# Kernel tuning notes

Measured on AMD Instinct MI355X. Metric: run time of the kernel, lower is better.

Reference implementation:

```python
import jax, jax.numpy as jnp
import numpy as np

H = 1024        # hidden_size
NH = 16         # num heads
HD = H // NH    # head dim = 64
B, S = 2, 2048


def _linear_params(key, fan_in, fan_out):
    k1, k2 = jax.random.split(key)
    bound = 1.0 / np.sqrt(fan_in)
    w = jax.random.uniform(k1, (fan_in, fan_out), jnp.float32, -bound, bound)
    b = jax.random.uniform(k2, (fan_out,), jnp.float32, -bound, bound)
    return w, b


def setup_inputs() -> dict:
    key = jax.random.key(0)
    ks = jax.random.split(key, 10)
    hidden_states = jax.random.normal(ks[0], (B, S, H), jnp.float32)
    topic_states = jax.random.normal(ks[1], (B, H), jnp.float32)
    attention_mask = jnp.zeros((B, 1, 1, S), jnp.float32)
    Wq, bq = _linear_params(ks[2], H, H)
    Wk, bk = _linear_params(ks[3], H, H)
    Wv, bv = _linear_params(ks[4], H, H)
    Wtp, btp = _linear_params(ks[5], H, H)
    Wta, bta = _linear_params(ks[6], H, H)
    Wd, bd = _linear_params(ks[7], H, H)
    ln_g = jnp.ones((H,), jnp.float32)
    ln_b = jnp.zeros((H,), jnp.float32)
    return {
        "hidden_states": hidden_states, "topic_states": topic_states,
        "attention_mask": attention_mask,
        "Wq": Wq, "bq": bq, "Wk": Wk, "bk": bk, "Wv": Wv, "bv": bv,
        "Wtp": Wtp, "btp": btp, "Wta": Wta, "bta": bta,
        "Wd": Wd, "bd": bd, "ln_g": ln_g, "ln_b": ln_b,
    }


def reference(hidden_states, topic_states, attention_mask,
              Wq, bq, Wk, bk, Wv, bv, Wtp, btp, Wta, bta, Wd, bd, ln_g, ln_b):
    # topic gating: two linears on [B,H], broadcast over seq
    topic_proj = topic_states @ Wtp + btp
    topic_att = topic_proj @ Wta + bta                     # [B,H]
    gate = jax.nn.sigmoid(topic_att)[:, None, :]           # [B,1,H]

    q = hidden_states @ Wq + bq                            # [B,S,H]
    k = (hidden_states @ Wk + bk) * gate                   # sigmoid-gated keys
    v = hidden_states @ Wv + bv

    def split_heads(x):  # [B,S,H] -> [B,NH,S,HD]
        return x.reshape(B, S, NH, HD).transpose(0, 2, 1, 3)

    qh, kh, vh = split_heads(q), split_heads(k), split_heads(v)

    scores = jnp.einsum('bhqd,bhkd->bhqk', qh, kh) / np.sqrt(HD).astype(np.float32)
    scores = scores + attention_mask                       # additive mask
    probs = jax.nn.softmax(scores, axis=-1)                # dropout = identity (eval)
    ctx = jnp.einsum('bhqk,bhkd->bhqd', probs, vh)
    ctx = ctx.transpose(0, 2, 1, 3).reshape(B, S, H)

    out = ctx @ Wd + bd                                    # dense + (eval) dropout
    x = out + hidden_states                                # residual
    mu = jnp.mean(x, axis=-1, keepdims=True)
    var = jnp.mean(jnp.square(x - mu), axis=-1, keepdims=True)
    return (x - mu) * jax.lax.rsqrt(var + 1e-5) * ln_g + ln_b
```

## Files before the change

kernel.cpp:

```cpp
#include <hip/hip_runtime.h>

typedef unsigned short u16;
typedef unsigned int   u32;
typedef __attribute__((ext_vector_type(4)))  float f32x4;
typedef __attribute__((ext_vector_type(16))) float f32x16;
typedef __attribute__((ext_vector_type(8)))  __bf16 bf16x8;
typedef __attribute__((ext_vector_type(8)))  u16  u16x8;
typedef __attribute__((ext_vector_type(4)))  u16  u16x4;

#define HDIM 1024
#define SEQ  2048
#define NB   2
#define MROWS 4096
#define QSCALE 0.18033688011111793f
#define LOG2E  1.4426950408889634f
#define TOPK 64
#define TOPC 16

__device__ __forceinline__ u16 f2bf(float f) {
  u32 u = __float_as_uint(f);
  u32 r = u + 0x7FFFu + ((u >> 16) & 1u);
  return (u16)(r >> 16);
}

__device__ __forceinline__ u32 pkbf(float a, float b) {
  union { __bf16 h[2]; u32 w; } u;
  u.h[0] = (__bf16)a; u.h[1] = (__bf16)b;
  return u.w;
}

__device__ __forceinline__ void gload_lds16(const void* gp, void* lp) {
  __builtin_amdgcn_global_load_lds(
      (const __attribute__((address_space(1))) void*)gp,
      (__attribute__((address_space(3))) void*)lp, 16, 0, 0);
}

__global__ void wt_bf16_kernel(const float* __restrict__ w0, const float* __restrict__ w1,
                               const float* __restrict__ w2, const float* __restrict__ w3,
                               u16* __restrict__ out) {
  const float* W = (blockIdx.z == 0) ? w0 : (blockIdx.z == 1) ? w1 : (blockIdx.z == 2) ? w2 : w3;
  u16* Wt = out + (size_t)blockIdx.z * HDIM * HDIM;
  __shared__ float t[32][33];
  const int k0 = blockIdx.x * 32, n0 = blockIdx.y * 32;
  const int tx = threadIdx.x, ty = threadIdx.y;
#pragma unroll
  for (int j = 0; j < 32; j += 8)
    t[ty + j][tx] = W[(size_t)(k0 + ty + j) * HDIM + n0 + tx];
  __syncthreads();
#pragma unroll
  for (int j = 0; j < 32; j += 8)
    Wt[(size_t)(n0 + ty + j) * HDIM + k0 + tx] = f2bf(t[tx][ty + j]);
}

__global__ void cvt_bf16_kernel(const float* __restrict__ in, u16* __restrict__ out) {
  const size_t i = (size_t)blockIdx.x * 256 + threadIdx.x;
  f32x4 v = *(const f32x4*)(in + i * 4);
  u16x4 o;
#pragma unroll
  for (int e = 0; e < 4; ++e) o[e] = f2bf(v[e]);
  *(u16x4*)(out + i * 4) = o;
}

__global__ void maskcvt_kernel(const float* __restrict__ m, float* __restrict__ o) {
  const int i = blockIdx.x * 256 + threadIdx.x;
  o[i] = m[i] * LOG2E;
}

__global__ void topic_partial_kernel(const float* __restrict__ in, const float* __restrict__ W,
                                     float* __restrict__ part) {
  const int c = blockIdx.x;
  const int b = blockIdx.y;
  const int t = threadIdx.x;
  const float* inb = in + b * HDIM + c * TOPK;
  f32x4 acc = {};
#pragma unroll 8
  for (int k = 0; k < TOPK; ++k) {
    const f32x4 w4 = *(const f32x4*)(W + (size_t)(c * TOPK + k) * HDIM + t * 4);
    acc += inb[k] * w4;
  }
  *(f32x4*)(part + ((size_t)(b * TOPC + c)) * HDIM + t * 4) = acc;
}

__global__ void topic_reduce_kernel(const float* __restrict__ part, const float* __restrict__ bias,
                                    float* __restrict__ out, int sigmoid_mode) {
  const int b = blockIdx.y;
  const int n = blockIdx.x * 256 + threadIdx.x;
  float s = bias[n];
#pragma unroll
  for (int c = 0; c < TOPC; ++c) s += part[((size_t)(b * TOPC + c)) * HDIM + n];
  out[b * HDIM + n] = sigmoid_mode ? (1.f / (1.f + __expf(-s))) : s;
}

template <int MODE>
__global__ __launch_bounds__(256, 2)
void gemm_kernel(const u16* __restrict__ A, const u16* __restrict__ Wt,
                 const float* __restrict__ b0, const float* __restrict__ b1,
                 const float* __restrict__ b2, const float* __restrict__ gate,
                 const float* __restrict__ resid,
                 u16* __restrict__ outb, float* __restrict__ outf) {
  const int n0 = blockIdx.x * 128;
  const int m0 = blockIdx.y * 128;
  const int z = blockIdx.z;
  const u16* W = Wt + (size_t)z * (HDIM * HDIM);
  const float* bias = (MODE == 0) ? (z == 0 ? b0 : (z == 1 ? b1 : b2)) : b0;

  __shared__ __align__(16) u16 Alds[128 * 64];
  __shared__ __align__(16) u16 Blds[128 * 64];

  const int tid = threadIdx.x;
  const int lane = tid & 63;
  const int w = tid >> 6;
  const int wm = w >> 1, wn = w & 1;
  const int srow = tid >> 3, sslot = tid & 7;

  f32x4 acc[4][4] = {};

  for (int k0 = 0; k0 < HDIM; k0 += 64) {
    __syncthreads();
#pragma unroll
    for (int j = 0; j < 4; ++j) {
      const int row = j * 32 + srow;
      const int gs = (sslot ^ (row & 7)) * 8;
      gload_lds16(A + (size_t)(m0 + row) * HDIM + k0 + gs, Alds + j * 2048 + w * 512);
      gload_lds16(W + (size_t)(n0 + row) * HDIM + k0 + gs, Blds + j * 2048 + w * 512);
    }
    __syncthreads();
#pragma unroll
    for (int kk = 0; kk < 2; ++kk) {
      const int slot = ((((kk << 2) + (lane >> 4)) ^ (lane & 7)) << 3);
      bf16x8 af[4], bfr[4];
#pragma unroll
      for (int i = 0; i < 4; ++i) {
        af[i]  = *(const bf16x8*)(&Alds[(wm * 64 + i * 16 + (lane & 15)) * 64 + slot]);
        bfr[i] = *(const bf16x8*)(&Blds[(wn * 64 + i * 16 + (lane & 15)) * 64 + slot]);
      }
#pragma unroll
      for (int i = 0; i < 4; ++i)
#pragma unroll
        for (int jn = 0; jn < 4; ++jn)
          acc[i][jn] = __builtin_amdgcn_mfma_f32_16x16x32_bf16(af[i], bfr[jn], acc[i][jn], 0, 0, 0);
    }
  }

  const int rbase = (lane >> 4) << 2;
#pragma unroll
  for (int i = 0; i < 4; ++i) {
#pragma unroll
    for (int jn = 0; jn < 4; ++jn) {
      const int n = n0 + wn * 64 + jn * 16 + (lane & 15);
      const float bv = bias[n];
#pragma unroll
      for (int r = 0; r < 4; ++r) {
        const int m = m0 + wm * 64 + i * 16 + rbase + r;
        float v = acc[i][jn][r] + bv;
        if (MODE == 0) {
          if (z == 0) v *= QSCALE;
          if (z == 1) v *= gate[(m >> 11) * HDIM + n];
          outb[(size_t)z * MROWS * HDIM + (size_t)m * HDIM + n] = f2bf(v);
        } else {
          v += resid[(size_t)m * HDIM + n];
          outf[(size_t)m * HDIM + n] = v;
        }
      }
    }
  }
}

__global__ __launch_bounds__(256, 2)
void attn_kernel(const u16* __restrict__ Q, const u16* __restrict__ K,
                 const u16* __restrict__ V, const float* __restrict__ mask2,
                 u16* __restrict__ O) {
  const int q0 = blockIdx.x * 128;
  const int h = blockIdx.y;
  const int b = blockIdx.z;
  const size_t base = ((size_t)b * SEQ) * HDIM + h * 64;
  const int tid = threadIdx.x, lane = tid & 63, w = tid >> 6;
  const int hh = lane >> 5;
  const int ql = lane & 31;
  const int srow = tid >> 3, sslot = tid & 7;

  __shared__ __align__(16) u16 Kss[2][64 * 64];
  __shared__ __align__(16) u16 Vts[2][64 * 64];

  bf16x8 Qf[4];
  {
    const u16* qp = Q + base + (size_t)(q0 + w * 32 + ql) * HDIM;
#pragma unroll
    for (int ds = 0; ds < 4; ++ds)
      Qf[ds] = *(const bf16x8*)(qp + ds * 16 + hh * 8);
  }

  float m_run = -1e30f, l_run = 0.f;
  f32x16 accA = {}, accB = {};

  {
#pragma unroll
    for (int c = 0; c < 2; ++c) {
      const int i2 = c * 4 + w;
      const int row = i2 * 8 + (lane >> 3);
      const int sl = lane & 7;
      gload_lds16(K + base + (size_t)row * HDIM + ((sl ^ (row & 7)) * 8),
                  &Kss[0][i2 * 512]);
    }
    u16x8 vr[2];
#pragma unroll
    for (int jj = 0; jj < 2; ++jj)
      vr[jj] = *(const u16x8*)(V + base + (size_t)(jj * 32 + srow) * HDIM + sslot * 8);
#pragma unroll
    for (int jj = 0; jj < 2; ++jj) {
      const int kr = jj * 32 + srow;
#pragma unroll
      for (int e = 0; e < 8; ++e) {
        const int d = sslot * 8 + e;
        Vts[0][d * 64 + ((((kr >> 3) ^ (d & 7) ^ ((d >> 3) & 7))) << 3) + (kr & 7)] = vr[jj][e];
      }
    }
  }
  __syncthreads();

  for (int t = 0; t < SEQ / 64; ++t) {
    const int cur = t & 1;
    const int kvt0 = t * 64;
    u16x8 vr[2];
    if (t + 1 < SEQ / 64) {
#pragma unroll
      for (int jj = 0; jj < 2; ++jj)
        vr[jj] = *(const u16x8*)(V + base + (size_t)(kvt0 + 64 + jj * 32 + srow) * HDIM + sslot * 8);
#pragma unroll
      for (int c = 0; c < 2; ++c) {
        const int i2 = c * 4 + w;
        const int row = i2 * 8 + (lane >> 3);
        const int sl = lane & 7;
        gload_lds16(K + base + (size_t)(kvt0 + 64 + row) * HDIM + ((sl ^ (row & 7)) * 8),
                    &Kss[cur ^ 1][i2 * 512]);
      }
    }

#pragma unroll
    for (int kvb = 0; kvb < 2; ++kvb) {
      f32x16 sv = {};
#pragma unroll
      for (int ds = 0; ds < 4; ++ds) {
        const bf16x8 kf = *(const bf16x8*)(
            &Kss[cur][(kvb * 32 + ql) * 64 + (((ds * 2 + hh) ^ (ql & 7)) << 3)]);
        sv = __builtin_amdgcn_mfma_f32_32x32x16_bf16(kf, Qf[ds], sv, 0, 0, 0);
      }
      f32x4 m4[4];
      {
        const float* mrow = mask2 + (size_t)b * SEQ + kvt0 + kvb * 32 + hh * 4;
#pragma unroll
        for (int g = 0; g < 4; ++g) m4[g] = *(const f32x4*)(mrow + g * 8);
      }
      f32x16 s_;
#pragma unroll
      for (int j = 0; j < 16; ++j) s_[j] = sv[j] + m4[j >> 2][j & 3];

      float mx0 = fmaxf(fmaxf(s_[0], s_[1]), fmaxf(s_[2], s_[3]));
      float mx1 = fmaxf(fmaxf(s_[4], s_[5]), fmaxf(s_[6], s_[7]));
      float mx2 = fmaxf(fmaxf(s_[8], s_[9]), fmaxf(s_[10], s_[11]));
      float mx3 = fmaxf(fmaxf(s_[12], s_[13]), fmaxf(s_[14], s_[15]));
      float mx = fmaxf(fmaxf(mx0, mx1), fmaxf(mx2, mx3));
      mx = fmaxf(mx, __shfl_xor(mx, 32));

      if (!__all(mx <= m_run + 8.f)) {
        const float mnew = fmaxf(m_run, mx);
        const float corr = __builtin_amdgcn_exp2f(m_run - mnew);
        m_run = mnew;
        l_run *= corr;
#pragma unroll
        for (int j = 0; j < 16; ++j) {
          const float cj = __shfl(corr, (j & 3) + 8 * (j >> 2) + 4 * hh);
          accA[j] *= cj; accB[j] *= cj;
        }
      }

      f32x16 p_;
#pragma unroll
      for (int j = 0; j < 16; ++j) p_[j] = __builtin_amdgcn_exp2f(s_[j] - m_run);
      {
        float r0 = (p_[0] + p_[1]) + (p_[2] + p_[3]);
        float r1 = (p_[4] + p_[5]) + (p_[6] + p_[7]);
        float r2 = (p_[8] + p_[9]) + (p_[10] + p_[11]);
        float r3 = (p_[12] + p_[13]) + (p_[14] + p_[15]);
        float rs = (r0 + r1) + (r2 + r3);
        rs += __shfl_xor(rs, 32);
        l_run += rs;
      }

#pragma unroll
      for (int s2 = 0; s2 < 2; ++s2) {
        const u32 a0 = pkbf(p_[s2 * 8 + 0], p_[s2 * 8 + 1]);
        const u32 a1 = pkbf(p_[s2 * 8 + 2], p_[s2 * 8 + 3]);
        const u32 b0v = pkbf(p_[s2 * 8 + 4], p_[s2 * 8 + 5]);
        const u32 b1v = pkbf(p_[s2 * 8 + 6], p_[s2 * 8 + 7]);
        const u32 sd0 = hh ? a0 : b0v, sd1 = hh ? a1 : b1v;
        const u32 r0 = (u32)__shfl_xor((int)sd0, 32);
        const u32 r1 = (u32)__shfl_xor((int)sd1, 32);
        union { u32 u[4]; bf16x8 v; } pu;
        pu.u[0] = hh ? r0 : a0;  pu.u[1] = hh ? r1 : a1;
        pu.u[2] = hh ? b0v : r0; pu.u[3] = hh ? b1v : r1;
        const int ks = kvb * 4 + s2 * 2 + hh;
#pragma unroll
        for (int dt = 0; dt < 2; ++dt) {
          const int d = dt * 32 + ql;
          const bf16x8 vf = *(const bf16x8*)(
              &Vts[cur][d * 64 + ((ks ^ (d & 7) ^ ((d >> 3) & 7)) << 3)]);
          if (dt == 0) accA = __builtin_amdgcn_mfma_f32_32x32x16_bf16(pu.v, vf, accA, 0, 0, 0);
          else         accB = __builtin_amdgcn_mfma_f32_32x32x16_bf16(pu.v, vf, accB, 0, 0, 0);
        }
      }
    }

    if (t + 1 < SEQ / 64) {
#pragma unroll
      for (int jj = 0; jj < 2; ++jj) {
        const int kr = jj * 32 + srow;
#pragma unroll
        for (int e = 0; e < 8; ++e) {
          const int d = sslot * 8 + e;
          Vts[cur ^ 1][d * 64 + ((((kr >> 3) ^ (d & 7) ^ ((d >> 3) & 7))) << 3) + (kr & 7)] = vr[jj][e];
        }
      }
    }
    __syncthreads();
  }

  const float linv = 1.f / l_run;
#pragma unroll
  for (int j = 0; j < 16; ++j) {
    const int rq = (j & 3) + 8 * (j >> 2) + 4 * hh;
    const float lj = __shfl(linv, rq);
    const size_t orow = base + (size_t)(q0 + w * 32 + rq) * HDIM;
    O[orow + ql]      = f2bf(accA[j] * lj);
    O[orow + 32 + ql] = f2bf(accB[j] * lj);
  }
}

__global__ void ln_kernel(const float* __restrict__ x, const float* __restrict__ g,
                          const float* __restrict__ bb, float* __restrict__ out) {
  const int row = blockIdx.x;
  const int tid = threadIdx.x;
  const f32x4 v = *(const f32x4*)(x + (size_t)row * HDIM + tid * 4);
  float s = v[0] + v[1] + v[2] + v[3];
  float s2 = v[0] * v[0] + v[1] * v[1] + v[2] * v[2] + v[3] * v[3];
#pragma unroll
  for (int o = 1; o < 64; o <<= 1) { s += __shfl_xor(s, o); s2 += __shfl_xor(s2, o); }
  __shared__ float rs[4], rs2[4];
  if ((tid & 63) == 0) { rs[tid >> 6] = s; rs2[tid >> 6] = s2; }
  __syncthreads();
  s = rs[0] + rs[1] + rs[2] + rs[3];
  s2 = rs2[0] + rs2[1] + rs2[2] + rs2[3];
  const float mu = s * (1.f / HDIM);
  const float var = s2 * (1.f / HDIM) - mu * mu;
  const float inv = rsqrtf(var + 1e-5f);
  f32x4 o4;
#pragma unroll
  for (int e = 0; e < 4; ++e) {
    const int c = tid * 4 + e;
    o4[e] = (v[e] - mu) * inv * g[c] + bb[c];
  }
  *(f32x4*)(out + (size_t)row * HDIM + tid * 4) = o4;
}

extern "C" void kernel_launch(void* const* d_in, const int* in_sizes, int n_in,
                              void* d_out, int out_size, void* d_ws, size_t ws_size,
                              hipStream_t stream) {
  const float* hidden = (const float*)d_in[0];
  const float* topic  = (const float*)d_in[1];
  const float* mask   = (const float*)d_in[2];
  const float* Wq  = (const float*)d_in[3];  const float* bq  = (const float*)d_in[4];
  const float* Wk  = (const float*)d_in[5];  const float* bk  = (const float*)d_in[6];
  const float* Wv  = (const float*)d_in[7];  const float* bv  = (const float*)d_in[8];
  const float* Wtp = (const float*)d_in[9];  const float* btp = (const float*)d_in[10];
  const float* Wta = (const float*)d_in[11]; const float* bta = (const float*)d_in[12];
  const float* Wd  = (const float*)d_in[13]; const float* bd  = (const float*)d_in[14];
  const float* lng = (const float*)d_in[15]; const float* lnb = (const float*)d_in[16];
  float* out = (float*)d_out;

  char* ws = (char*)d_ws;
  u16* hs_bf  = (u16*)(ws);
  u16* WtAll  = (u16*)(ws + (size_t)(8u << 20));
  u16* qkv    = (u16*)(ws + (size_t)(16u << 20));
  u16* ctx    = (u16*)(ws + (size_t)(40u << 20));
  float* xbuf = (float*)(ws + (size_t)(16u << 20));
  float* tproj = (float*)(ws + (size_t)(48u << 20));
  float* tgate = (float*)(ws + (size_t)(48u << 20) + 8192);
  float* mask2 = (float*)(ws + (size_t)(48u << 20));
  float* tpart = (float*)(ws + (size_t)(16u << 20));

  wt_bf16_kernel<<<dim3(32, 32, 4), dim3(32, 8), 0, stream>>>(Wq, Wk, Wv, Wd, WtAll);
  cvt_bf16_kernel<<<4096, 256, 0, stream>>>(hidden, hs_bf);
  topic_partial_kernel<<<dim3(TOPC, NB), 256, 0, stream>>>(topic, Wtp, tpart);
  topic_reduce_kernel<<<dim3(4, NB), 256, 0, stream>>>(tpart, btp, tproj, 0);
  topic_partial_kernel<<<dim3(TOPC, NB), 256, 0, stream>>>(tproj, Wta, tpart);
  topic_reduce_kernel<<<dim3(4, NB), 256, 0, stream>>>(tpart, bta, tgate, 1);
  gemm_kernel<0><<<dim3(8, 32, 3), 256, 0, stream>>>(hs_bf, WtAll, bq, bk, bv, tgate,
                                                     nullptr, qkv, nullptr);
  maskcvt_kernel<<<16, 256, 0, stream>>>(mask, mask2);
  attn_kernel<<<dim3(16, 16, NB), 256, 0, stream>>>(qkv, qkv + (size_t)MROWS * HDIM,
                                                    qkv + 2 * (size_t)MROWS * HDIM, mask2, ctx);
  gemm_kernel<1><<<dim3(8, 32, 1), 256, 0, stream>>>(ctx, WtAll + 3 * (size_t)HDIM * HDIM,
                                                     bd, nullptr, nullptr, nullptr, hidden,
                                                     nullptr, xbuf);
  ln_kernel<<<4096, 256, 0, stream>>>(xbuf, lng, lnb, out);
}
```

Measured before the change: 163.9 us.

## Process full 64-key tile per softmax step, fold mask scaling, add MFMA priority

```diff
diff --git a/kernel.cpp b/kernel.cpp
--- a/kernel.cpp
+++ b/kernel.cpp
@@ -59,11 +59,6 @@
 #pragma unroll
   for (int e = 0; e < 4; ++e) o[e] = f2bf(v[e]);
   *(u16x4*)(out + i * 4) = o;
-}
-
-__global__ void maskcvt_kernel(const float* __restrict__ m, float* __restrict__ o) {
-  const int i = blockIdx.x * 256 + threadIdx.x;
-  o[i] = m[i] * LOG2E;
 }
 
 __global__ void topic_partial_kernel(const float* __restrict__ in, const float* __restrict__ W,
@@ -168,7 +163,7 @@
 
 __global__ __launch_bounds__(256, 2)
 void attn_kernel(const u16* __restrict__ Q, const u16* __restrict__ K,
-                 const u16* __restrict__ V, const float* __restrict__ mask2,
+                 const u16* __restrict__ V, const float* __restrict__ mask,
                  u16* __restrict__ O) {
   const int q0 = blockIdx.x * 128;
   const int h = blockIdx.y;
@@ -236,63 +231,82 @@
       }
     }
 
+    f32x16 sv[2] = {{}, {}};
+    __builtin_amdgcn_s_setprio(1);
+#pragma unroll
+    for (int ds = 0; ds < 4; ++ds) {
+      const int xo = (((ds * 2 + hh) ^ (ql & 7)) << 3);
+      const bf16x8 kf0 = *(const bf16x8*)(&Kss[cur][(ql) * 64 + xo]);
+      const bf16x8 kf1 = *(const bf16x8*)(&Kss[cur][(32 + ql) * 64 + xo]);
+      sv[0] = __builtin_amdgcn_mfma_f32_32x32x16_bf16(kf0, Qf[ds], sv[0], 0, 0, 0);
+      sv[1] = __builtin_amdgcn_mfma_f32_32x32x16_bf16(kf1, Qf[ds], sv[1], 0, 0, 0);
+    }
+    __builtin_amdgcn_s_setprio(0);
+
+    f32x4 m4[2][4];
+    {
+      const float* mrow = mask + (size_t)b * SEQ + kvt0 + hh * 4;
+#pragma unroll
+      for (int g = 0; g < 4; ++g) {
+        m4[0][g] = *(const f32x4*)(mrow + g * 8);
+        m4[1][g] = *(const f32x4*)(mrow + 32 + g * 8);
+      }
+    }
+    f32x16 s_[2];
+#pragma unroll
+    for (int kvb = 0; kvb < 2; ++kvb)
+#pragma unroll
+      for (int j = 0; j < 16; ++j)
+        s_[kvb][j] = fmaf(m4[kvb][j >> 2][j & 3], LOG2E, sv[kvb][j]);
+
+    float t8[8];
+#pragma unroll
+    for (int j = 0; j < 8; ++j)
+      t8[j] = fmaxf(fmaxf(s_[0][j], s_[0][j + 8]), fmaxf(s_[1][j], s_[1][j + 8]));
+    float t4a = fmaxf(t8[0], t8[1]), t4b = fmaxf(t8[2], t8[3]);
+    float t4c = fmaxf(t8[4], t8[5]), t4d = fmaxf(t8[6], t8[7]);
+    float mx = fmaxf(fmaxf(t4a, t4b), fmaxf(t4c, t4d));
+    mx = fmaxf(mx, __shfl_xor(mx, 32));
+
+    if (!__all(mx <= m_run + 8.f)) {
+      const float mnew = fmaxf(m_run, mx);
+      const float corr = __builtin_amdgcn_exp2f(m_run - mnew);
+      m_run = mnew;
+      l_run *= corr;
+#pragma unroll
+      for (int j = 0; j < 16; ++j) {
+        const float cj = __shfl(corr, (j & 3) + 8 * (j >> 2) + 4 * hh);
+        accA[j] *= cj; accB[j] *= cj;
+      }
+    }
+
+    f32x16 p_[2];
+#pragma unroll
+    for (int kvb = 0; kvb < 2; ++kvb)
+#pragma unroll
+      for (int j = 0; j < 16; ++j)
+        p_[kvb][j] = __builtin_amdgcn_exp2f(s_[kvb][j] - m_run);
+    {
+      float r8[8];
+#pragma unroll
+      for (int j = 0; j < 8; ++j)
+        r8[j] = (p_[0][j] + p_[0][j + 8]) + (p_[1][j] + p_[1][j + 8]);
+      float ra = (r8[0] + r8[1]) + (r8[2] + r8[3]);
+      float rb = (r8[4] + r8[5]) + (r8[6] + r8[7]);
+      float rs = ra + rb;
+      rs += __shfl_xor(rs, 32);
+      l_run += rs;
+    }
+
+    __builtin_amdgcn_s_setprio(1);
 #pragma unroll
     for (int kvb = 0; kvb < 2; ++kvb) {
-      f32x16 sv = {};
-#pragma unroll
-      for (int ds = 0; ds < 4; ++ds) {
-        const bf16x8 kf = *(const bf16x8*)(
-            &Kss[cur][(kvb * 32 + ql) * 64 + (((ds * 2 + hh) ^ (ql & 7)) << 3)]);
-        sv = __builtin_amdgcn_mfma_f32_32x32x16_bf16(kf, Qf[ds], sv, 0, 0, 0);
-      }
-      f32x4 m4[4];
-      {
-        const float* mrow = mask2 + (size_t)b * SEQ + kvt0 + kvb * 32 + hh * 4;
-#pragma unroll
-        for (int g = 0; g < 4; ++g) m4[g] = *(const f32x4*)(mrow + g * 8);
-      }
-      f32x16 s_;
-#pragma unroll
-      for (int j = 0; j < 16; ++j) s_[j] = sv[j] + m4[j >> 2][j & 3];
-
-      float mx0 = fmaxf(fmaxf(s_[0], s_[1]), fmaxf(s_[2], s_[3]));
-      float mx1 = fmaxf(fmaxf(s_[4], s_[5]), fmaxf(s_[6], s_[7]));
-      float mx2 = fmaxf(fmaxf(s_[8], s_[9]), fmaxf(s_[10], s_[11]));
-      float mx3 = fmaxf(fmaxf(s_[12], s_[13]), fmaxf(s_[14], s_[15]));
-      float mx = fmaxf(fmaxf(mx0, mx1), fmaxf(mx2, mx3));
-      mx = fmaxf(mx, __shfl_xor(mx, 32));
-
-      if (!__all(mx <= m_run + 8.f)) {
-        const float mnew = fmaxf(m_run, mx);
-        const float corr = __builtin_amdgcn_exp2f(m_run - mnew);
-        m_run = mnew;
-        l_run *= corr;
-#pragma unroll
-        for (int j = 0; j < 16; ++j) {
-          const float cj = __shfl(corr, (j & 3) + 8 * (j >> 2) + 4 * hh);
-          accA[j] *= cj; accB[j] *= cj;
-        }
-      }
-
-      f32x16 p_;
-#pragma unroll
-      for (int j = 0; j < 16; ++j) p_[j] = __builtin_amdgcn_exp2f(s_[j] - m_run);
-      {
-        float r0 = (p_[0] + p_[1]) + (p_[2] + p_[3]);
-        float r1 = (p_[4] + p_[5]) + (p_[6] + p_[7]);
-        float r2 = (p_[8] + p_[9]) + (p_[10] + p_[11]);
-        float r3 = (p_[12] + p_[13]) + (p_[14] + p_[15]);
-        float rs = (r0 + r1) + (r2 + r3);
-        rs += __shfl_xor(rs, 32);
-        l_run += rs;
-      }
-
 #pragma unroll
       for (int s2 = 0; s2 < 2; ++s2) {
-        const u32 a0 = pkbf(p_[s2 * 8 + 0], p_[s2 * 8 + 1]);
-        const u32 a1 = pkbf(p_[s2 * 8 + 2], p_[s2 * 8 + 3]);
-        const u32 b0v = pkbf(p_[s2 * 8 + 4], p_[s2 * 8 + 5]);
-        const u32 b1v = pkbf(p_[s2 * 8 + 6], p_[s2 * 8 + 7]);
+        const u32 a0 = pkbf(p_[kvb][s2 * 8 + 0], p_[kvb][s2 * 8 + 1]);
+        const u32 a1 = pkbf(p_[kvb][s2 * 8 + 2], p_[kvb][s2 * 8 + 3]);
+        const u32 b0v = pkbf(p_[kvb][s2 * 8 + 4], p_[kvb][s2 * 8 + 5]);
+        const u32 b1v = pkbf(p_[kvb][s2 * 8 + 6], p_[kvb][s2 * 8 + 7]);
         const u32 sd0 = hh ? a0 : b0v, sd1 = hh ? a1 : b1v;
         const u32 r0 = (u32)__shfl_xor((int)sd0, 32);
         const u32 r1 = (u32)__shfl_xor((int)sd1, 32);
@@ -310,6 +324,7 @@
         }
       }
     }
+    __builtin_amdgcn_s_setprio(0);
 
     if (t + 1 < SEQ / 64) {
 #pragma unroll
@@ -385,7 +400,6 @@
   float* xbuf = (float*)(ws + (size_t)(16u << 20));
   float* tproj = (float*)(ws + (size_t)(48u << 20));
   float* tgate = (float*)(ws + (size_t)(48u << 20) + 8192);
-  float* mask2 = (float*)(ws + (size_t)(48u << 20));
   float* tpart = (float*)(ws + (size_t)(16u << 20));
 
   wt_bf16_kernel<<<dim3(32, 32, 4), dim3(32, 8), 0, stream>>>(Wq, Wk, Wv, Wd, WtAll);
@@ -396,9 +410,8 @@
   topic_reduce_kernel<<<dim3(4, NB), 256, 0, stream>>>(tpart, bta, tgate, 1);
   gemm_kernel<0><<<dim3(8, 32, 3), 256, 0, stream>>>(hs_bf, WtAll, bq, bk, bv, tgate,
                                                      nullptr, qkv, nullptr);
-  maskcvt_kernel<<<16, 256, 0, stream>>>(mask, mask2);
   attn_kernel<<<dim3(16, 16, NB), 256, 0, stream>>>(qkv, qkv + (size_t)MROWS * HDIM,
-                                                    qkv + 2 * (size_t)MROWS * HDIM, mask2, ctx);
+                                                    qkv + 2 * (size_t)MROWS * HDIM, mask, ctx);
   gemm_kernel<1><<<dim3(8, 32, 1), 256, 0, stream>>>(ctx, WtAll + 3 * (size_t)HDIM * HDIM,
                                                      bd, nullptr, nullptr, nullptr, hidden,
                                                      nullptr, xbuf);
```

Measured after the change: 165.4 us. Within noise of the previous version (+0.9%).

## Pre-transpose V in global memory and async-load K/V tiles into LDS

Applied to the files above, without the earlier changes.

```diff
diff --git a/kernel.cpp b/kernel.cpp
--- a/kernel.cpp
+++ b/kernel.cpp
@@ -59,11 +59,6 @@
 #pragma unroll
   for (int e = 0; e < 4; ++e) o[e] = f2bf(v[e]);
   *(u16x4*)(out + i * 4) = o;
-}
-
-__global__ void maskcvt_kernel(const float* __restrict__ m, float* __restrict__ o) {
-  const int i = blockIdx.x * 256 + threadIdx.x;
-  o[i] = m[i] * LOG2E;
 }
 
 __global__ void topic_partial_kernel(const float* __restrict__ in, const float* __restrict__ W,
@@ -166,18 +161,42 @@
   }
 }
 
+__global__ void vtrans_kernel(const u16* __restrict__ v, u16* __restrict__ vt) {
+  const int s0 = blockIdx.x * 64, h = blockIdx.y, b = blockIdx.z;
+  __shared__ u16 T[64][66];
+  const int tid = threadIdx.x;
+  const int r = tid >> 3, c8 = (tid & 7) * 8;
+#pragma unroll
+  for (int p = 0; p < 2; ++p) {
+    const int srow = p * 32 + r;
+    const u16x8 val = *(const u16x8*)(v + (size_t)(b * SEQ + s0 + srow) * HDIM + h * 64 + c8);
+#pragma unroll
+    for (int e = 0; e < 8; ++e) T[srow][c8 + e] = val[e];
+  }
+  __syncthreads();
+#pragma unroll
+  for (int p = 0; p < 2; ++p) {
+    const int drow = p * 32 + r;
+    u16x8 o;
+#pragma unroll
+    for (int e = 0; e < 8; ++e) o[e] = T[c8 + e][drow];
+    *(u16x8*)(vt + (size_t)((b * 16 + h) * 64 + drow) * SEQ + s0 + c8) = o;
+  }
+}
+
 __global__ __launch_bounds__(256, 2)
 void attn_kernel(const u16* __restrict__ Q, const u16* __restrict__ K,
-                 const u16* __restrict__ V, const float* __restrict__ mask2,
+                 const u16* __restrict__ Vt, const float* __restrict__ mask,
                  u16* __restrict__ O) {
   const int q0 = blockIdx.x * 128;
   const int h = blockIdx.y;
   const int b = blockIdx.z;
   const size_t base = ((size_t)b * SEQ) * HDIM + h * 64;
+  const size_t vtbase = (size_t)((b * 16 + h) * 64) * SEQ;
   const int tid = threadIdx.x, lane = tid & 63, w = tid >> 6;
   const int hh = lane >> 5;
   const int ql = lane & 31;
-  const int srow = tid >> 3, sslot = tid & 7;
+  const int NT = SEQ / 64;
 
   __shared__ __align__(16) u16 Kss[2][64 * 64];
   __shared__ __align__(16) u16 Vts[2][64 * 64];
@@ -190,70 +209,61 @@
       Qf[ds] = *(const bf16x8*)(qp + ds * 16 + hh * 8);
   }
 
+  const int l3 = lane >> 3, l7 = lane & 7;
+  const u16* ksrc0 = K + base + (size_t)(w * 8 + l3) * HDIM + ((l7 ^ l3) << 3);
+  const u16* ksrc1 = K + base + (size_t)((4 + w) * 8 + l3) * HDIM + ((l7 ^ l3) << 3);
+  const u16* vsrc0 = Vt + vtbase + (size_t)(w * 16 + l3) * SEQ + (((l7 ^ l3 ^ (w * 2)) & 7) << 3);
+  const u16* vsrc1 = Vt + vtbase + (size_t)(w * 16 + 8 + l3) * SEQ + (((l7 ^ l3 ^ (w * 2 + 1)) & 7) << 3);
+
+  const u16* kaddr[4];
+#pragma unroll
+  for (int ds = 0; ds < 4; ++ds)
+    kaddr[ds] = &Kss[0][ql * 64 + (((ds * 2 + hh) ^ (ql & 7)) << 3)];
+  const u16* vaddr[2][4];
+#pragma unroll
+  for (int dt = 0; dt < 2; ++dt) {
+    const int d = dt * 32 + ql;
+    const int sw = (d & 7) ^ ((d >> 3) & 7);
+#pragma unroll
+    for (int c = 0; c < 4; ++c)
+      vaddr[dt][c] = &Vts[0][d * 64 + (((c * 2 + hh) ^ sw) << 3)];
+  }
+
   float m_run = -1e30f, l_run = 0.f;
   f32x16 accA = {}, accB = {};
 
-  {
-#pragma unroll
-    for (int c = 0; c < 2; ++c) {
-      const int i2 = c * 4 + w;
-      const int row = i2 * 8 + (lane >> 3);
-      const int sl = lane & 7;
-      gload_lds16(K + base + (size_t)row * HDIM + ((sl ^ (row & 7)) * 8),
-                  &Kss[0][i2 * 512]);
-    }
-    u16x8 vr[2];
-#pragma unroll
-    for (int jj = 0; jj < 2; ++jj)
-      vr[jj] = *(const u16x8*)(V + base + (size_t)(jj * 32 + srow) * HDIM + sslot * 8);
-#pragma unroll
-    for (int jj = 0; jj < 2; ++jj) {
-      const int kr = jj * 32 + srow;
-#pragma unroll
-      for (int e = 0; e < 8; ++e) {
-        const int d = sslot * 8 + e;
-        Vts[0][d * 64 + ((((kr >> 3) ^ (d & 7) ^ ((d >> 3) & 7))) << 3) + (kr & 7)] = vr[jj][e];
-      }
-    }
-  }
+  auto STAGE = [&](int ncur, int t1) {
+    const size_t ko = (size_t)(t1 * 64) * HDIM;
+    const int vo = t1 * 64;
+    gload_lds16(ksrc0 + ko, &Kss[ncur][w * 512]);
+    gload_lds16(ksrc1 + ko, &Kss[ncur][(4 + w) * 512]);
+    gload_lds16(vsrc0 + vo, &Vts[ncur][w * 1024]);
+    gload_lds16(vsrc1 + vo, &Vts[ncur][w * 1024 + 512]);
+  };
+
+  STAGE(0, 0);
   __syncthreads();
 
-  for (int t = 0; t < SEQ / 64; ++t) {
-    const int cur = t & 1;
+  auto BODY = [&](int t, const int cur) {
+    if (t + 1 < NT) STAGE(cur ^ 1, t + 1);
     const int kvt0 = t * 64;
-    u16x8 vr[2];
-    if (t + 1 < SEQ / 64) {
-#pragma unroll
-      for (int jj = 0; jj < 2; ++jj)
-        vr[jj] = *(const u16x8*)(V + base + (size_t)(kvt0 + 64 + jj * 32 + srow) * HDIM + sslot * 8);
-#pragma unroll
-      for (int c = 0; c < 2; ++c) {
-        const int i2 = c * 4 + w;
-        const int row = i2 * 8 + (lane >> 3);
-        const int sl = lane & 7;
-        gload_lds16(K + base + (size_t)(kvt0 + 64 + row) * HDIM + ((sl ^ (row & 7)) * 8),
-                    &Kss[cur ^ 1][i2 * 512]);
-      }
-    }
-
 #pragma unroll
     for (int kvb = 0; kvb < 2; ++kvb) {
       f32x16 sv = {};
 #pragma unroll
       for (int ds = 0; ds < 4; ++ds) {
-        const bf16x8 kf = *(const bf16x8*)(
-            &Kss[cur][(kvb * 32 + ql) * 64 + (((ds * 2 + hh) ^ (ql & 7)) << 3)]);
+        const bf16x8 kf = *(const bf16x8*)(kaddr[ds] + cur * 4096 + kvb * 2048);
         sv = __builtin_amdgcn_mfma_f32_32x32x16_bf16(kf, Qf[ds], sv, 0, 0, 0);
       }
       f32x4 m4[4];
       {
-        const float* mrow = mask2 + (size_t)b * SEQ + kvt0 + kvb * 32 + hh * 4;
+        const float* mrow = mask + (size_t)b * SEQ + kvt0 + kvb * 32 + hh * 4;
 #pragma unroll
         for (int g = 0; g < 4; ++g) m4[g] = *(const f32x4*)(mrow + g * 8);
       }
       f32x16 s_;
 #pragma unroll
-      for (int j = 0; j < 16; ++j) s_[j] = sv[j] + m4[j >> 2][j & 3];
+      for (int j = 0; j < 16; ++j) s_[j] = fmaf(m4[j >> 2][j & 3], LOG2E, sv[j]);
 
       float mx0 = fmaxf(fmaxf(s_[0], s_[1]), fmaxf(s_[2], s_[3]));
       float mx1 = fmaxf(fmaxf(s_[4], s_[5]), fmaxf(s_[6], s_[7]));
@@ -299,30 +309,19 @@
         union { u32 u[4]; bf16x8 v; } pu;
         pu.u[0] = hh ? r0 : a0;  pu.u[1] = hh ? r1 : a1;
         pu.u[2] = hh ? b0v : r0; pu.u[3] = hh ? b1v : r1;
-        const int ks = kvb * 4 + s2 * 2 + hh;
-#pragma unroll
-        for (int dt = 0; dt < 2; ++dt) {
-          const int d = dt * 32 + ql;
-          const bf16x8 vf = *(const bf16x8*)(
-              &Vts[cur][d * 64 + ((ks ^ (d & 7) ^ ((d >> 3) & 7)) << 3)]);
-          if (dt == 0) accA = __builtin_amdgcn_mfma_f32_32x32x16_bf16(pu.v, vf, accA, 0, 0, 0);
-          else         accB = __builtin_amdgcn_mfma_f32_32x32x16_bf16(pu.v, vf, accB, 0, 0, 0);
-        }
-      }
-    }
-
-    if (t + 1 < SEQ / 64) {
-#pragma unroll
-      for (int jj = 0; jj < 2; ++jj) {
-        const int kr = jj * 32 + srow;
-#pragma unroll
-        for (int e = 0; e < 8; ++e) {
-          const int d = sslot * 8 + e;
-          Vts[cur ^ 1][d * 64 + ((((kr >> 3) ^ (d & 7) ^ ((d >> 3) & 7))) << 3) + (kr & 7)] = vr[jj][e];
-        }
+        const int c = kvb * 2 + s2;
+        const bf16x8 vf0 = *(const bf16x8*)(vaddr[0][c] + cur * 4096);
+        const bf16x8 vf1 = *(const bf16x8*)(vaddr[1][c] + cur * 4096);
+        accA = __builtin_amdgcn_mfma_f32_32x32x16_bf16(pu.v, vf0, accA, 0, 0, 0);
+        accB = __builtin_amdgcn_mfma_f32_32x32x16_bf16(pu.v, vf1, accB, 0, 0, 0);
       }
     }
     __syncthreads();
+  };
+
+  for (int tt = 0; tt < NT; tt += 2) {
+    BODY(tt, 0);
+    BODY(tt + 1, 1);
   }
 
   const float linv = 1.f / l_run;
@@ -382,10 +381,10 @@
   u16* WtAll  = (u16*)(ws + (size_t)(8u << 20));
   u16* qkv    = (u16*)(ws + (size_t)(16u << 20));
   u16* ctx    = (u16*)(ws + (size_t)(40u << 20));
+  u16* VtG    = (u16*)(ws + (size_t)(48u << 20));
   float* xbuf = (float*)(ws + (size_t)(16u << 20));
-  float* tproj = (float*)(ws + (size_t)(48u << 20));
-  float* tgate = (float*)(ws + (size_t)(48u << 20) + 8192);
-  float* mask2 = (float*)(ws + (size_t)(48u << 20));
+  float* tproj = (float*)(ws + (size_t)(64u << 20));
+  float* tgate = (float*)(ws + (size_t)(64u << 20) + 8192);
   float* tpart = (float*)(ws + (size_t)(16u << 20));
 
   wt_bf16_kernel<<<dim3(32, 32, 4), dim3(32, 8), 0, stream>>>(Wq, Wk, Wv, Wd, WtAll);
@@ -396,9 +395,9 @@
   topic_reduce_kernel<<<dim3(4, NB), 256, 0, stream>>>(tpart, bta, tgate, 1);
   gemm_kernel<0><<<dim3(8, 32, 3), 256, 0, stream>>>(hs_bf, WtAll, bq, bk, bv, tgate,
                                                      nullptr, qkv, nullptr);
-  maskcvt_kernel<<<16, 256, 0, stream>>>(mask, mask2);
+  vtrans_kernel<<<dim3(32, 16, NB), 256, 0, stream>>>(qkv + 2 * (size_t)MROWS * HDIM, VtG);
   attn_kernel<<<dim3(16, 16, NB), 256, 0, stream>>>(qkv, qkv + (size_t)MROWS * HDIM,
-                                                    qkv + 2 * (size_t)MROWS * HDIM, mask2, ctx);
+                                                    VtG, mask, ctx);
   gemm_kernel<1><<<dim3(8, 32, 1), 256, 0, stream>>>(ctx, WtAll + 3 * (size_t)HDIM * HDIM,
                                                      bd, nullptr, nullptr, nullptr, hidden,
                                                      nullptr, xbuf);
```

After: 166.3 us. Within noise of the previous version (+1.5%).
